# Optimization experiments

Hardware: AMD Instinct MI355X
Metric: run time of the kernel (lower is better)

Reference implementation:

```python
import jax, jax.numpy as jnp
import numpy as np

HEADS = 4
KD = 32          # key_dim per head
LEVELS = 2
G = 3            # 2**dims - 1 HP orientation groups
STRENGTH = 0.25
DECAY = 0.6
LN_EPS = 1e-5
MIX_EPS = 1e-3


def _layernorm(x, g, b):
    m = jnp.mean(x, axis=-1, keepdims=True)
    v = jnp.var(x, axis=-1, keepdims=True)
    return (x - m) * jax.lax.rsqrt(v + LN_EPS) * g + b


def _dwt2(x):
    # Haar analysis, periodic/even sizes. [B,H,W,C] -> [B,H/2,W/2,4C] (LL,LH,HL,HH)
    x00 = x[:, 0::2, 0::2]; x01 = x[:, 0::2, 1::2]
    x10 = x[:, 1::2, 0::2]; x11 = x[:, 1::2, 1::2]
    ll = (x00 + x01 + x10 + x11) * 0.5
    lh = (x00 - x01 + x10 - x11) * 0.5
    hl = (x00 + x01 - x10 - x11) * 0.5
    hh = (x00 - x01 - x10 + x11) * 0.5
    return jnp.concatenate([ll, lh, hl, hh], axis=-1)


def _idwt2(w):
    # exact Haar synthesis: [B,H/2,W/2,4C] -> [B,H,W,C]
    ll, lh, hl, hh = jnp.split(w, 4, axis=-1)
    x00 = (ll + lh + hl + hh) * 0.5
    x01 = (ll - lh + hl - hh) * 0.5
    x10 = (ll + lh - hl - hh) * 0.5
    x11 = (ll - lh - hl + hh) * 0.5
    B, H2, W2, C = ll.shape
    r0 = jnp.stack([x00, x01], axis=3).reshape(B, H2, 2 * W2, C)  # interleave W
    r1 = jnp.stack([x10, x11], axis=3).reshape(B, H2, 2 * W2, C)
    return jnp.stack([r0, r1], axis=2).reshape(B, 2 * H2, 2 * W2, C)  # interleave H


def _axial_mhsa(x, p):
    # AxialMHSAND: sequential sweep over spatial axes; each pass is
    # proj(attn(softmax(QK^T/sqrt(d)) V)) on norm(x), qkv via 1x1 conv (=matmul).
    g, b, wq, bq, wk, bk, wv, bv, wp, bp = p
    scale = KD ** -0.5
    for axis in (1, 2):
        X = _layernorm(x, g, b)
        B, H, W, _ = X.shape
        Q = (X @ wq + bq).reshape(B, H, W, HEADS, KD)
        K = (X @ wk + bk).reshape(B, H, W, HEADS, KD)
        V = (X @ wv + bv).reshape(B, H, W, HEADS, KD)
        if axis == 1:  # attend along H, batch over (B, W, heads)
            A = jax.nn.softmax(jnp.einsum('bqwnd,bkwnd->bwnqk', Q, K) * scale, axis=-1)
            Y = jnp.einsum('bwnqk,bkwnd->bqwnd', A, V)
        else:          # attend along W, batch over (B, H, heads)
            A = jax.nn.softmax(jnp.einsum('bhqnd,bhknd->bhnqk', Q, K) * scale, axis=-1)
            Y = jnp.einsum('bhnqk,bhknd->bhqnd', A, V)
        x = Y.reshape(B, H, W, HEADS * KD) @ wp + bp
    return x


def setup_inputs() -> dict:
    key = jax.random.key(0)
    ks = jax.random.split(key, 24)
    C = 64
    HD = HEADS * KD
    s = 0.02
    inp = {'x': jax.random.normal(ks[0], (4, 256, 256, C), jnp.float32)}
    i = 1
    for pre in ('lp', 'hp'):
        inp[pre + '_ln_g'] = jnp.ones((C,), jnp.float32)
        inp[pre + '_ln_b'] = jnp.zeros((C,), jnp.float32)
        inp[pre + '_wq'] = jax.random.normal(ks[i], (C, HD), jnp.float32) * s
        inp[pre + '_bq'] = jax.random.normal(ks[i + 1], (HD,), jnp.float32) * s
        inp[pre + '_wk'] = jax.random.normal(ks[i + 2], (C, HD), jnp.float32) * s
        inp[pre + '_bk'] = jax.random.normal(ks[i + 3], (HD,), jnp.float32) * s
        inp[pre + '_wv'] = jax.random.normal(ks[i + 4], (C, HD), jnp.float32) * s
        inp[pre + '_bv'] = jax.random.normal(ks[i + 5], (HD,), jnp.float32) * s
        inp[pre + '_wp'] = jax.random.normal(ks[i + 6], (HD, C), jnp.float32) * s
        inp[pre + '_bp'] = jax.random.normal(ks[i + 7], (C,), jnp.float32) * s
        i += 8
    mix = jnp.eye(G, dtype=jnp.float32) + MIX_EPS * (jnp.ones((G, G), jnp.float32) - jnp.eye(G, dtype=jnp.float32))
    inp['mix_w0'] = mix
    inp['mix_w1'] = mix
    return inp


def reference(x, lp_ln_g, lp_ln_b, lp_wq, lp_bq, lp_wk, lp_bk, lp_wv, lp_bv, lp_wp, lp_bp,
              hp_ln_g, hp_ln_b, hp_wq, hp_bq, hp_wk, hp_bk, hp_wv, hp_bv, hp_wp, hp_bp,
              mix_w0, mix_w1):
    lp_p = (lp_ln_g, lp_ln_b, lp_wq, lp_bq, lp_wk, lp_bk, lp_wv, lp_bv, lp_wp, lp_bp)
    hp_p = (hp_ln_g, hp_ln_b, hp_wq, hp_bq, hp_wk, hp_bk, hp_wv, hp_bv, hp_wp, hp_bp)
    mix_ws = [mix_w0, mix_w1]
    C = x.shape[-1]
    cur = x
    hps = []
    for _ in range(LEVELS):  # analysis pyramid
        w = _dwt2(cur)
        hps.append(w[..., C:])
        cur = w[..., :C]
    # deepest LP: axial attention, residual with full strength
    cur = cur + STRENGTH * _axial_mhsa(cur, lp_p)
    for l in reversed(range(LEVELS)):  # synthesis with per-level HP processing
        hp = hps[l]
        B, H2, W2, _ = hp.shape
        gain = STRENGTH * (DECAY ** (LEVELS - 1 - l))  # coarser levels stronger
        hp_g = hp.reshape(B, H2, W2, G, C)
        mixed = jnp.einsum('gd,bhwdc->bhwgc', mix_ws[l], hp_g)  # OrientationMix
        batched = mixed.transpose(3, 0, 1, 2, 4).reshape(G * B, H2, W2, C)
        att = _axial_mhsa(batched, hp_p)  # shared hp_attn across groups/levels
        att = att.reshape(G, B, H2, W2, C).transpose(1, 2, 3, 0, 4).reshape(B, H2, W2, G * C)
        hp_out = hp + gain * att
        cur = _idwt2(jnp.concatenate([cur, hp_out], axis=-1))
    return cur
```

## Files before the change

kernel.cpp:

```cpp
#include <hip/hip_runtime.h>

#define LN_EPS 1e-5f
#define QSCALE 0.25500526578425445f

typedef __attribute__((ext_vector_type(8))) short bf16x8;
typedef __attribute__((ext_vector_type(4))) float f32x4;

#define MFMA16(A, B, C) __builtin_amdgcn_mfma_f32_16x16x32_bf16(A, B, C, 0, 0, 0)

static __device__ __forceinline__ unsigned short f2bf_rne(float f) {
    union { unsigned int i; float f; } c; c.f = f;
    unsigned int i = c.i;
    return (unsigned short)((i + 0x7fffu + ((i >> 16) & 1u)) >> 16);
}
static __device__ __forceinline__ void bfstore2(unsigned short* p, float x, float y) {
    *(unsigned int*)p = (unsigned int)f2bf_rne(x) | ((unsigned int)f2bf_rne(y) << 16);
}
static __device__ __forceinline__ unsigned pk2(float a, float b) {
    return __builtin_amdgcn_perm(__builtin_bit_cast(unsigned, b),
                                 __builtin_bit_cast(unsigned, a), 0x07060302u);
}
static __device__ __forceinline__ unsigned short tb16(float f) {
    return (unsigned short)(__builtin_bit_cast(unsigned, f) >> 16);
}
static __device__ __forceinline__ float bftrunc(float f) {
    return __builtin_bit_cast(float, __builtin_bit_cast(unsigned, f) & 0xFFFF0000u);
}

__global__ void dwt_kernel(const float4* __restrict__ in, float4* __restrict__ ll,
                           float4* __restrict__ hp, int B, int H2, int W2) {
    const int i = blockIdx.x * blockDim.x + threadIdx.x;
    const int total = B * H2 * W2 * 16;
    if (i >= total) return;
    const int c4 = i & 15;
    int t = i >> 4;
    const int w2 = t % W2; t /= W2;
    const int h2 = t % H2;
    const int b = t / H2;
    const int W = W2 * 2;
    const size_t base = (((size_t)b * (H2 * 2) + 2 * h2) * W + 2 * w2) * 16 + c4;
    const float4 x00 = in[base];
    const float4 x01 = in[base + 16];
    const float4 x10 = in[base + (size_t)W * 16];
    const float4 x11 = in[base + (size_t)W * 16 + 16];
    float4 vll, vlh, vhl, vhh;
#define DWTC(a) \
    vll.a = (x00.a + x01.a + x10.a + x11.a) * 0.5f; \
    vlh.a = (x00.a - x01.a + x10.a - x11.a) * 0.5f; \
    vhl.a = (x00.a + x01.a - x10.a - x11.a) * 0.5f; \
    vhh.a = (x00.a - x01.a - x10.a + x11.a) * 0.5f;
    DWTC(x) DWTC(y) DWTC(z) DWTC(w)
#undef DWTC
    const size_t oi = ((size_t)b * H2 + h2) * W2 + w2;
    ll[oi * 16 + c4] = vll;
    hp[oi * 48 + c4] = vlh;
    hp[oi * 48 + 16 + c4] = vhl;
    hp[oi * 48 + 32 + c4] = vhh;
}

__global__ void idwt_kernel(const float4* __restrict__ cur, const float4* __restrict__ hp,
                            const float4* __restrict__ att, float gain,
                            float4* __restrict__ out, int B, int H2, int W2) {
    const int i = blockIdx.x * blockDim.x + threadIdx.x;
    const int total = B * H2 * W2 * 16;
    if (i >= total) return;
    const int c4 = i & 15;
    int t = i >> 4;
    const int w2 = t % W2; t /= W2;
    const int h2 = t % H2;
    const int b = t / H2;
    const size_t oi = ((size_t)b * H2 + h2) * W2 + w2;
    const size_t sp = (size_t)h2 * W2 + w2;
    const size_t gstr = (size_t)B * H2 * W2;
    const float4 vll = cur[oi * 16 + c4];
    float4 vlh = hp[oi * 48 + c4];
    float4 vhl = hp[oi * 48 + 16 + c4];
    float4 vhh = hp[oi * 48 + 32 + c4];
    const float4 a0 = att[((size_t)b * H2 * W2 + sp) * 16 + c4];
    const float4 a1 = att[((size_t)b * H2 * W2 + gstr + sp) * 16 + c4];
    const float4 a2 = att[((size_t)b * H2 * W2 + 2 * gstr + sp) * 16 + c4];
#define ADDG(a) \
    vlh.a = fmaf(gain, a0.a, vlh.a); \
    vhl.a = fmaf(gain, a1.a, vhl.a); \
    vhh.a = fmaf(gain, a2.a, vhh.a);
    ADDG(x) ADDG(y) ADDG(z) ADDG(w)
#undef ADDG
    float4 x00, x01, x10, x11;
#define IDWTC(a) \
    x00.a = (vll.a + vlh.a + vhl.a + vhh.a) * 0.5f; \
    x01.a = (vll.a - vlh.a + vhl.a - vhh.a) * 0.5f; \
    x10.a = (vll.a + vlh.a - vhl.a - vhh.a) * 0.5f; \
    x11.a = (vll.a - vlh.a - vhl.a + vhh.a) * 0.5f;
    IDWTC(x) IDWTC(y) IDWTC(z) IDWTC(w)
#undef IDWTC
    const int W = W2 * 2;
    const size_t r0 = (((size_t)b * (H2 * 2) + 2 * h2) * W + 2 * w2) * 16 + c4;
    out[r0] = x00;
    out[r0 + 16] = x01;
    out[r0 + (size_t)W * 16] = x10;
    out[r0 + (size_t)W * 16 + 16] = x11;
}

__global__ void prep_weights(const float* __restrict__ lwq, const float* __restrict__ lwk,
                             const float* __restrict__ lwv, const float* __restrict__ lwp,
                             const float* __restrict__ hwq, const float* __restrict__ hwk,
                             const float* __restrict__ hwv, const float* __restrict__ hwp,
                             unsigned short* __restrict__ wbuf) {
    const int i = blockIdx.x * blockDim.x + threadIdx.x;
    if (i >= 65536) return;
    const int set = i >> 15;
    const int r = i & 32767;
    const float* wq = set ? hwq : lwq;
    const float* wk = set ? hwk : lwk;
    const float* wv = set ? hwv : lwv;
    const float* wp = set ? hwp : lwp;
    float v;
    if (r < 24576) {
        const int nn = r >> 6, c = r & 63;
        const float* w = (nn < 128) ? wq : (nn < 256) ? wk : wv;
        v = w[c * 128 + (nn & 127)];
        if (nn < 128) v *= QSCALE;
    } else {
        const int r2 = r - 24576;
        const int nn = r2 >> 7, d = r2 & 127;
        v = wp[d * 64 + nn];
    }
    wbuf[i] = f2bf_rne(v);
}

struct Job {
    const float* xin;
    const float* mixsrc;
    const float* mixw;
    float* xout;
    const float* basep;
    float res_scale;
    const float* ln_g; const float* ln_b;
    const float* bq; const float* bk; const float* bv; const float* bp;
    const unsigned short* wqkvT;
    const unsigned short* wpT;
};

template<int S>
__global__ __launch_bounds__(512, 4)
void axial_attn(Job jA, Job jB, int nA, int axis)
{
    constexpr int BS = 512;
    constexpr int CK = 32;
    constexpr int NCH = S / CK;
    constexpr int NSI = S / 32;
    constexpr int CSTR = 40;

    __shared__ __align__(16) unsigned short Xs[S * 64];
    __shared__ __align__(16) unsigned short Arena[18432];

    const int tid = threadIdx.x;
    const int lane = tid & 63;
    const int w = tid >> 6;
    const int n16 = lane & 15;
    const int quad = lane >> 4;

    const bool isB = (int)blockIdx.x >= nA;
    const Job j = isB ? jB : jA;
    const int line = isB ? (int)blockIdx.x - nA : (int)blockIdx.x;
    const int lb = line / S;
    const int lr = line - lb * S;
    size_t lbase, tstr;
    if (axis == 1) { lbase = ((size_t)lb * S * S + lr) * 64; tstr = (size_t)S * 64; }
    else           { lbase = ((size_t)lb * S + lr) * (size_t)S * 64; tstr = 64; }

    const bf16x8 Wk0 = *(const bf16x8*)&j.wqkvT[((8 + w) * 16 + n16) * 64 + quad * 8];
    const bf16x8 Wk1 = *(const bf16x8*)&j.wqkvT[((8 + w) * 16 + n16) * 64 + 32 + quad * 8];
    const bf16x8 Wv0 = *(const bf16x8*)&j.wqkvT[((16 + w) * 16 + n16) * 64 + quad * 8];
    const bf16x8 Wv1 = *(const bf16x8*)&j.wqkvT[((16 + w) * 16 + n16) * 64 + 32 + quad * 8];
    const float bk = j.bk[w * 16 + n16];
    const float bv = j.bv[w * 16 + n16];

    {
        const int sub = tid & 15;
        const float4 g4 = ((const float4*)j.ln_g)[sub];
        const float4 be4 = ((const float4*)j.ln_b)[sub];
        const float4* x4 = (const float4*)j.xin;
        const float4* hp4 = (const float4*)j.mixsrc;
        const size_t lbase4 = lbase >> 2, tstr4 = tstr >> 2;
        float m0, m1, m2; int bimg;
        if (hp4) {
            const int g = lb >> 2;
            bimg = lb & 3;
            m0 = j.mixw[g * 3 + 0]; m1 = j.mixw[g * 3 + 1]; m2 = j.mixw[g * 3 + 2];
        }
        for (int t = (tid >> 4); t < S; t += BS / 16) {
            float4 v;
            if (hp4) {
                const int pos = (axis == 1) ? (t * S + lr) : (lr * S + t);
                const size_t hb = ((size_t)bimg * S * S + pos) * 48 + sub;
                const float4 h0 = hp4[hb];
                const float4 h1 = hp4[hb + 16];
                const float4 h2 = hp4[hb + 32];
                v.x = m0 * h0.x + m1 * h1.x + m2 * h2.x;
                v.y = m0 * h0.y + m1 * h1.y + m2 * h2.y;
                v.z = m0 * h0.z + m1 * h1.z + m2 * h2.z;
                v.w = m0 * h0.w + m1 * h1.w + m2 * h2.w;
            } else {
                v = x4[lbase4 + (size_t)t * tstr4 + sub];
            }
            float s = v.x + v.y + v.z + v.w;
            float ss = v.x * v.x + v.y * v.y + v.z * v.z + v.w * v.w;
            #pragma unroll
            for (int m = 1; m < 16; m <<= 1) {
                s += __shfl_xor(s, m);
                ss += __shfl_xor(ss, m);
            }
            const float mean = s * 0.015625f;
            const float rstd = rsqrtf(ss * 0.015625f - mean * mean + LN_EPS);
            unsigned short* xr = &Xs[(t << 6) + ((sub * 4) ^ ((t & 7) << 3))];
            bfstore2(xr,     (v.x - mean) * rstd * g4.x + be4.x,
                             (v.y - mean) * rstd * g4.y + be4.y);
            bfstore2(xr + 2, (v.z - mean) * rstd * g4.z + be4.z,
                             (v.w - mean) * rstd * g4.w + be4.w);
        }
    }
    __syncthreads();

    {
        const float bias = j.bq[w * 16 + n16] * QSCALE;
        const bf16x8 Bq0 = *(const bf16x8*)&j.wqkvT[(w * 16 + n16) * 64 + quad * 8];
        const bf16x8 Bq1 = *(const bf16x8*)&j.wqkvT[(w * 16 + n16) * 64 + 32 + quad * 8];
        #pragma unroll
        for (int mt = 0; mt < S / 16; ++mt) {
            const int xr = mt * 16 + n16;
            const int xm = (xr & 7) << 3;
            const bf16x8 A0 = *(const bf16x8*)&Xs[(xr << 6) + ((quad * 8) ^ xm)];
            const bf16x8 A1 = *(const bf16x8*)&Xs[(xr << 6) + ((32 + quad * 8) ^ xm)];
            f32x4 acc = {bias, bias, bias, bias};
            acc = MFMA16(A0, Bq0, acc);
            acc = MFMA16(A1, Bq1, acc);
            const int row0 = mt * 16 + quad * 4;
            #pragma unroll
            for (int r = 0; r < 4; ++r) {
                const int rr = row0 + r;
                Arena[(rr << 7) + ((w * 16 + n16) ^ ((rr & 7) << 3))] = tb16(acc[r]);
            }
        }
    }
    __syncthreads();

    const int h = w >> 1;
    const int sub = w & 1;
    const int hoff = h * 32;

    bf16x8 qb[NSI];
    #pragma unroll
    for (int si = 0; si < NSI; ++si) {
        const int qr = (sub * NSI + si) * 16 + n16;
        qb[si] = *(const bf16x8*)&Arena[(qr << 7) + ((hoff + quad * 8) ^ ((qr & 7) << 3))];
    }
    f32x4 y0[NSI], y1[NSI];
    float rsum[NSI];
    #pragma unroll
    for (int si = 0; si < NSI; ++si) {
        y0[si] = (f32x4){0.f, 0.f, 0.f, 0.f};
        y1[si] = (f32x4){0.f, 0.f, 0.f, 0.f};
        rsum[si] = 0.f;
    }
    __syncthreads();

    auto produce = [&](int kc, int buf) {
        const int k0 = kc * CK;
        unsigned short* Kc = &Arena[buf * 4096];
        unsigned short* Vc = &Arena[8192 + buf * 5120];
        #pragma unroll
        for (int mtl = 0; mtl < 2; ++mtl) {
            const int xr = k0 + mtl * 16 + n16;
            const int xm = (xr & 7) << 3;
            const bf16x8 A0 = *(const bf16x8*)&Xs[(xr << 6) + ((quad * 8) ^ xm)];
            const bf16x8 A1 = *(const bf16x8*)&Xs[(xr << 6) + ((32 + quad * 8) ^ xm)];
            f32x4 ak = {bk, bk, bk, bk};
            ak = MFMA16(A0, Wk0, ak);
            ak = MFMA16(A1, Wk1, ak);
            const int row0 = mtl * 16 + quad * 4;
            #pragma unroll
            for (int r = 0; r < 4; ++r) {
                const int rr = row0 + r;
                Kc[(rr << 7) + ((w * 16 + n16) ^ ((rr & 7) << 3))] = tb16(ak[r]);
            }
            f32x4 av = {bv, bv, bv, bv};
            av = MFMA16(A0, Wv0, av);
            av = MFMA16(A1, Wv1, av);
            *(uint2*)&Vc[(w * 16 + n16) * CSTR + mtl * 16 + quad * 4] =
                make_uint2(pk2(av[0], av[1]), pk2(av[2], av[3]));
        }
    };

    const int sr0 = ((n16 >> 2) << 3) + (n16 & 3);
    const int sr1 = sr0 + 4;

    produce(0, 0);
    __syncthreads();
    for (int kc = 0; kc < NCH; ++kc) {
        const int buf = kc & 1;
        const unsigned short* Kc = &Arena[buf * 4096];
        const unsigned short* Vc = &Arena[8192 + buf * 5120];
        const bf16x8 ka0 = *(const bf16x8*)&Kc[(sr0 << 7) + ((hoff + quad * 8) ^ ((sr0 & 7) << 3))];
        const bf16x8 ka1 = *(const bf16x8*)&Kc[(sr1 << 7) + ((hoff + quad * 8) ^ ((sr1 & 7) << 3))];
        const bf16x8 vb0 = *(const bf16x8*)&Vc[(hoff + n16) * CSTR + quad * 8];
        const bf16x8 vb1 = *(const bf16x8*)&Vc[(hoff + 16 + n16) * CSTR + quad * 8];
        if (kc + 1 < NCH) produce(kc + 1, buf ^ 1);
        #pragma unroll
        for (int si = 0; si < NSI; ++si) {
            f32x4 sc0 = {0.f, 0.f, 0.f, 0.f};
            f32x4 sc1 = {0.f, 0.f, 0.f, 0.f};
            sc0 = MFMA16(ka0, qb[si], sc0);
            sc1 = MFMA16(ka1, qb[si], sc1);
            const float e0 = __builtin_amdgcn_exp2f(sc0[0]);
            const float e1 = __builtin_amdgcn_exp2f(sc0[1]);
            const float e2 = __builtin_amdgcn_exp2f(sc0[2]);
            const float e3 = __builtin_amdgcn_exp2f(sc0[3]);
            const float e4 = __builtin_amdgcn_exp2f(sc1[0]);
            const float e5 = __builtin_amdgcn_exp2f(sc1[1]);
            const float e6 = __builtin_amdgcn_exp2f(sc1[2]);
            const float e7 = __builtin_amdgcn_exp2f(sc1[3]);
            rsum[si] += ((bftrunc(e0) + bftrunc(e1)) + (bftrunc(e2) + bftrunc(e3)))
                      + ((bftrunc(e4) + bftrunc(e5)) + (bftrunc(e6) + bftrunc(e7)));
            union { unsigned u[4]; bf16x8 v; } pau;
            pau.u[0] = pk2(e0, e1);
            pau.u[1] = pk2(e2, e3);
            pau.u[2] = pk2(e4, e5);
            pau.u[3] = pk2(e6, e7);
            y0[si] = MFMA16(pau.v, vb0, y0[si]);
            y1[si] = MFMA16(pau.v, vb1, y1[si]);
        }
        __syncthreads();
    }

    #pragma unroll
    for (int si = 0; si < NSI; ++si) {
        float red = rsum[si];
        red += __shfl_xor(red, 16);
        red += __shfl_xor(red, 32);
        const int q0 = (sub * NSI + si) * 16;
        #pragma unroll
        for (int r = 0; r < 4; ++r) {
            const float inv = __builtin_amdgcn_rcpf(__shfl(red, quad * 4 + r));
            const int row = q0 + quad * 4 + r;
            const int m = (row & 7) << 3;
            Arena[(row << 7) + ((hoff + n16) ^ m)]      = tb16(y0[si][r] * inv);
            Arena[(row << 7) + ((hoff + 16 + n16) ^ m)] = tb16(y1[si][r] * inv);
        }
    }
    __syncthreads();

    {
        constexpr int TD = (S / 16) * 4 / 8;
        const int mt = (w * TD) >> 2;
        const int nt0 = (w * TD) & 3;
        const int m0 = mt * 16;
        const int ym = (n16 & 7) << 3;
        bf16x8 pa[4];
        #pragma unroll
        for (int kt = 0; kt < 4; ++kt)
            pa[kt] = *(const bf16x8*)&Arena[((m0 + n16) << 7) + ((kt * 32 + quad * 8) ^ ym)];
        #pragma unroll
        for (int i = 0; i < TD; ++i) {
            const int nt = nt0 + i;
            const float bias = j.bp[nt * 16 + n16];
            f32x4 acc = {bias, bias, bias, bias};
            #pragma unroll
            for (int kt = 0; kt < 4; ++kt) {
                const bf16x8 wb = *(const bf16x8*)&j.wpT[(nt * 16 + n16) * 128 + kt * 32 + quad * 8];
                acc = MFMA16(pa[kt], wb, acc);
            }
            #pragma unroll
            for (int r = 0; r < 4; ++r) {
                const size_t gi = lbase + (size_t)(m0 + quad * 4 + r) * tstr + nt * 16 + n16;
                float v = acc[r];
                if (j.basep) v = fmaf(j.res_scale, v, j.basep[gi]);
                j.xout[gi] = v;
            }
        }
    }
}

extern "C" void kernel_launch(void* const* d_in, const int* in_sizes, int n_in,
                              void* d_out, int out_size, void* d_ws, size_t ws_size,
                              hipStream_t stream) {
    (void)in_sizes; (void)n_in; (void)out_size; (void)ws_size;
    const float* x = (const float*)d_in[0];
    const float* P_lp[10];
    const float* P_hp[10];
    for (int i = 0; i < 10; ++i) P_lp[i] = (const float*)d_in[1 + i];
    for (int i = 0; i < 10; ++i) P_hp[i] = (const float*)d_in[11 + i];
    const float* mw0 = (const float*)d_in[21];
    const float* mw1 = (const float*)d_in[22];
    float* out = (float*)d_out;
    float* ws = (float*)d_ws;

    float* ll0 = ws;
    float* hp0 = ll0 + (size_t)4194304;
    float* t0  = hp0 + (size_t)12582912;
    float* ll1  = t0;
    float* hp1  = t0 + (size_t)1048576;
    float* ta2  = t0 + (size_t)4194304;
    float* lpta = t0 + (size_t)7340032;
    float* tb  = out;
    float* t1b = out;
    unsigned short* wbuf = (unsigned short*)(out + (size_t)13631488);

    prep_weights<<<256, 256, 0, stream>>>(
        P_lp[2], P_lp[4], P_lp[6], P_lp[8],
        P_hp[2], P_hp[4], P_hp[6], P_hp[8], wbuf);

    dwt_kernel<<<4 * 128 * 128 * 16 / 256, 256, 0, stream>>>(
        (const float4*)x, (float4*)ll0, (float4*)hp0, 4, 128, 128);
    dwt_kernel<<<4 * 64 * 64 * 16 / 256, 256, 0, stream>>>(
        (const float4*)ll0, (float4*)ll1, (float4*)hp1, 4, 64, 64);

    const unsigned short* lp_qkvT = wbuf;
    const unsigned short* lp_wpT  = wbuf + 24576;
    const unsigned short* hp_qkvT = wbuf + 32768;
    const unsigned short* hp_wpT  = wbuf + 32768 + 24576;

    auto mkjob = [](const float* xin, const float* mixsrc, const float* mixw,
                    float* xout, const float* basep, float rs,
                    const float* const* P, const unsigned short* qkvT,
                    const unsigned short* wpT) {
        Job jj;
        jj.xin = xin; jj.mixsrc = mixsrc; jj.mixw = mixw;
        jj.xout = xout; jj.basep = basep; jj.res_scale = rs;
        jj.ln_g = P[0]; jj.ln_b = P[1];
        jj.bq = P[3]; jj.bk = P[5]; jj.bv = P[7]; jj.bp = P[9];
        jj.wqkvT = qkvT; jj.wpT = wpT;
        return jj;
    };

    {
        Job a1 = mkjob(ll1, nullptr, nullptr, lpta, nullptr, 1.f, P_lp, lp_qkvT, lp_wpT);
        Job b1 = mkjob(nullptr, hp1, mw1, tb, nullptr, 1.f, P_hp, hp_qkvT, hp_wpT);
        axial_attn<64><<<1024, 512, 0, stream>>>(a1, b1, 256, 1);
        Job a2 = mkjob(lpta, nullptr, nullptr, ll1, ll1, 0.25f, P_lp, lp_qkvT, lp_wpT);
        Job b2 = mkjob(tb, nullptr, nullptr, ta2, nullptr, 1.f, P_hp, hp_qkvT, hp_wpT);
        axial_attn<64><<<1024, 512, 0, stream>>>(a2, b2, 256, 2);
    }
    idwt_kernel<<<4 * 64 * 64 * 16 / 256, 256, 0, stream>>>(
        (const float4*)ll1, (const float4*)hp1, (const float4*)ta2, 0.25f,
        (float4*)ll0, 4, 64, 64);

    {
        Job c1 = mkjob(nullptr, hp0, mw0, t1b, nullptr, 1.f, P_hp, hp_qkvT, hp_wpT);
        axial_attn<128><<<1536, 512, 0, stream>>>(c1, c1, 1536, 1);
        Job c2 = mkjob(t1b, nullptr, nullptr, t0, nullptr, 1.f, P_hp, hp_qkvT, hp_wpT);
        axial_attn<128><<<1536, 512, 0, stream>>>(c2, c2, 1536, 2);
    }
    idwt_kernel<<<4 * 128 * 128 * 16 / 256, 256, 0, stream>>>(
        (const float4*)ll0, (const float4*)hp0, (const float4*)t0, 0.15f,
        (float4*)out, 4, 128, 128);
}
```

Measured before the change: 398.6 us.

## Make each wave compute its own head's Q/K/V to drop block barriers

Each wave now projects Q, K and V only for its own head's 32 columns into a private shared-memory slice. This replaces the shared, double-buffered K/V production that needed a block-wide __syncthreads per chunk. The waves sharing a head now compute the same K/V redundantly, which doubles K/V MFMA work, and the produce step no longer overlaps with attention. The Y staging buffer moves to a padded row layout in place of the XOR swizzle.

After: 467.8 us. +17.4%, slower.

```diff
diff --git a/kernel.cpp b/kernel.cpp
--- a/kernel.cpp
+++ b/kernel.cpp
@@ -146,13 +146,12 @@
 void axial_attn(Job jA, Job jB, int nA, int axis)
 {
     constexpr int BS = 512;
-    constexpr int CK = 32;
-    constexpr int NCH = S / CK;
     constexpr int NSI = S / 32;
-    constexpr int CSTR = 40;
+    constexpr int NCH = S / 32;
+    constexpr int SLICE = 2304;
 
     __shared__ __align__(16) unsigned short Xs[S * 64];
-    __shared__ __align__(16) unsigned short Arena[18432];
+    __shared__ __align__(16) unsigned short Arena[8 * SLICE];
 
     const int tid = threadIdx.x;
     const int lane = tid & 63;
@@ -169,12 +168,12 @@
     if (axis == 1) { lbase = ((size_t)lb * S * S + lr) * 64; tstr = (size_t)S * 64; }
     else           { lbase = ((size_t)lb * S + lr) * (size_t)S * 64; tstr = 64; }
 
-    const bf16x8 Wk0 = *(const bf16x8*)&j.wqkvT[((8 + w) * 16 + n16) * 64 + quad * 8];
-    const bf16x8 Wk1 = *(const bf16x8*)&j.wqkvT[((8 + w) * 16 + n16) * 64 + 32 + quad * 8];
-    const bf16x8 Wv0 = *(const bf16x8*)&j.wqkvT[((16 + w) * 16 + n16) * 64 + quad * 8];
-    const bf16x8 Wv1 = *(const bf16x8*)&j.wqkvT[((16 + w) * 16 + n16) * 64 + 32 + quad * 8];
-    const float bk = j.bk[w * 16 + n16];
-    const float bv = j.bv[w * 16 + n16];
+    const int hh = w >> 1;
+    const int qhalf = w & 1;
+    const int qbase = qhalf * (S / 2);
+    unsigned short* Qw = &Arena[w * SLICE];
+    unsigned short* Kw = &Arena[w * SLICE];
+    unsigned short* Vw = &Arena[w * SLICE + 1024];
 
     {
         const int sub = tid & 15;
@@ -222,39 +221,40 @@
     }
     __syncthreads();
 
-    {
-        const float bias = j.bq[w * 16 + n16] * QSCALE;
-        const bf16x8 Bq0 = *(const bf16x8*)&j.wqkvT[(w * 16 + n16) * 64 + quad * 8];
-        const bf16x8 Bq1 = *(const bf16x8*)&j.wqkvT[(w * 16 + n16) * 64 + 32 + quad * 8];
-        #pragma unroll
-        for (int mt = 0; mt < S / 16; ++mt) {
-            const int xr = mt * 16 + n16;
-            const int xm = (xr & 7) << 3;
-            const bf16x8 A0 = *(const bf16x8*)&Xs[(xr << 6) + ((quad * 8) ^ xm)];
-            const bf16x8 A1 = *(const bf16x8*)&Xs[(xr << 6) + ((32 + quad * 8) ^ xm)];
+    #pragma unroll
+    for (int si = 0; si < NSI; ++si) {
+        const int xr = qbase + si * 16 + n16;
+        const int xm = (xr & 7) << 3;
+        const bf16x8 A0 = *(const bf16x8*)&Xs[(xr << 6) + ((quad * 8) ^ xm)];
+        const bf16x8 A1 = *(const bf16x8*)&Xs[(xr << 6) + ((32 + quad * 8) ^ xm)];
+        #pragma unroll
+        for (int c = 0; c < 2; ++c) {
+            const int nt = 2 * hh + c;
+            const float bias = j.bq[nt * 16 + n16] * QSCALE;
+            const bf16x8 B0 = *(const bf16x8*)&j.wqkvT[(nt * 16 + n16) * 64 + quad * 8];
+            const bf16x8 B1 = *(const bf16x8*)&j.wqkvT[(nt * 16 + n16) * 64 + 32 + quad * 8];
             f32x4 acc = {bias, bias, bias, bias};
-            acc = MFMA16(A0, Bq0, acc);
-            acc = MFMA16(A1, Bq1, acc);
-            const int row0 = mt * 16 + quad * 4;
+            acc = MFMA16(A0, B0, acc);
+            acc = MFMA16(A1, B1, acc);
             #pragma unroll
             for (int r = 0; r < 4; ++r) {
-                const int rr = row0 + r;
-                Arena[(rr << 7) + ((w * 16 + n16) ^ ((rr & 7) << 3))] = tb16(acc[r]);
-            }
-        }
-    }
-    __syncthreads();
-
-    const int h = w >> 1;
-    const int sub = w & 1;
-    const int hoff = h * 32;
+                const int lrow = si * 16 + quad * 4 + r;
+                const int col = c * 16 + n16;
+                Qw[lrow * 32 + ((((col >> 3) ^ (lrow & 3)) << 3) | (col & 7))] = tb16(acc[r]);
+            }
+        }
+    }
+    asm volatile("s_waitcnt lgkmcnt(0)" ::: "memory");
 
     bf16x8 qb[NSI];
     #pragma unroll
     for (int si = 0; si < NSI; ++si) {
-        const int qr = (sub * NSI + si) * 16 + n16;
-        qb[si] = *(const bf16x8*)&Arena[(qr << 7) + ((hoff + quad * 8) ^ ((qr & 7) << 3))];
-    }
+        const int lrow = si * 16 + n16;
+        qb[si] = *(const bf16x8*)&Qw[lrow * 32 + ((quad ^ (lrow & 3)) << 3)];
+    }
+    asm volatile("s_waitcnt lgkmcnt(0)" ::: "memory");
+    __builtin_amdgcn_sched_barrier(0);
+
     f32x4 y0[NSI], y1[NSI];
     float rsum[NSI];
     #pragma unroll
@@ -263,49 +263,59 @@
         y1[si] = (f32x4){0.f, 0.f, 0.f, 0.f};
         rsum[si] = 0.f;
     }
-    __syncthreads();
-
-    auto produce = [&](int kc, int buf) {
-        const int k0 = kc * CK;
-        unsigned short* Kc = &Arena[buf * 4096];
-        unsigned short* Vc = &Arena[8192 + buf * 5120];
+    const int sr0 = ((n16 >> 2) << 3) + (n16 & 3);
+    const int sr1 = sr0 + 4;
+
+    for (int kc = 0; kc < NCH; ++kc) {
+        const int k0 = kc * 32;
+        bf16x8 A[2][2];
         #pragma unroll
         for (int mtl = 0; mtl < 2; ++mtl) {
             const int xr = k0 + mtl * 16 + n16;
             const int xm = (xr & 7) << 3;
-            const bf16x8 A0 = *(const bf16x8*)&Xs[(xr << 6) + ((quad * 8) ^ xm)];
-            const bf16x8 A1 = *(const bf16x8*)&Xs[(xr << 6) + ((32 + quad * 8) ^ xm)];
-            f32x4 ak = {bk, bk, bk, bk};
-            ak = MFMA16(A0, Wk0, ak);
-            ak = MFMA16(A1, Wk1, ak);
-            const int row0 = mtl * 16 + quad * 4;
-            #pragma unroll
-            for (int r = 0; r < 4; ++r) {
-                const int rr = row0 + r;
-                Kc[(rr << 7) + ((w * 16 + n16) ^ ((rr & 7) << 3))] = tb16(ak[r]);
-            }
-            f32x4 av = {bv, bv, bv, bv};
-            av = MFMA16(A0, Wv0, av);
-            av = MFMA16(A1, Wv1, av);
-            *(uint2*)&Vc[(w * 16 + n16) * CSTR + mtl * 16 + quad * 4] =
-                make_uint2(pk2(av[0], av[1]), pk2(av[2], av[3]));
-        }
-    };
-
-    const int sr0 = ((n16 >> 2) << 3) + (n16 & 3);
-    const int sr1 = sr0 + 4;
-
-    produce(0, 0);
-    __syncthreads();
-    for (int kc = 0; kc < NCH; ++kc) {
-        const int buf = kc & 1;
-        const unsigned short* Kc = &Arena[buf * 4096];
-        const unsigned short* Vc = &Arena[8192 + buf * 5120];
-        const bf16x8 ka0 = *(const bf16x8*)&Kc[(sr0 << 7) + ((hoff + quad * 8) ^ ((sr0 & 7) << 3))];
-        const bf16x8 ka1 = *(const bf16x8*)&Kc[(sr1 << 7) + ((hoff + quad * 8) ^ ((sr1 & 7) << 3))];
-        const bf16x8 vb0 = *(const bf16x8*)&Vc[(hoff + n16) * CSTR + quad * 8];
-        const bf16x8 vb1 = *(const bf16x8*)&Vc[(hoff + 16 + n16) * CSTR + quad * 8];
-        if (kc + 1 < NCH) produce(kc + 1, buf ^ 1);
+            A[mtl][0] = *(const bf16x8*)&Xs[(xr << 6) + ((quad * 8) ^ xm)];
+            A[mtl][1] = *(const bf16x8*)&Xs[(xr << 6) + ((32 + quad * 8) ^ xm)];
+        }
+        #pragma unroll
+        for (int c = 0; c < 2; ++c) {
+            const int nt = 8 + 2 * hh + c;
+            const float bias = j.bk[(2 * hh + c) * 16 + n16];
+            const bf16x8 W0 = *(const bf16x8*)&j.wqkvT[(nt * 16 + n16) * 64 + quad * 8];
+            const bf16x8 W1 = *(const bf16x8*)&j.wqkvT[(nt * 16 + n16) * 64 + 32 + quad * 8];
+            #pragma unroll
+            for (int mtl = 0; mtl < 2; ++mtl) {
+                f32x4 ak = {bias, bias, bias, bias};
+                ak = MFMA16(A[mtl][0], W0, ak);
+                ak = MFMA16(A[mtl][1], W1, ak);
+                #pragma unroll
+                for (int r = 0; r < 4; ++r) {
+                    const int key = mtl * 16 + quad * 4 + r;
+                    const int col = c * 16 + n16;
+                    Kw[key * 32 + ((((col >> 3) ^ (key & 3)) << 3) | (col & 7))] = tb16(ak[r]);
+                }
+            }
+        }
+        #pragma unroll
+        for (int c = 0; c < 2; ++c) {
+            const int nt = 16 + 2 * hh + c;
+            const float bias = j.bv[(2 * hh + c) * 16 + n16];
+            const bf16x8 W0 = *(const bf16x8*)&j.wqkvT[(nt * 16 + n16) * 64 + quad * 8];
+            const bf16x8 W1 = *(const bf16x8*)&j.wqkvT[(nt * 16 + n16) * 64 + 32 + quad * 8];
+            #pragma unroll
+            for (int mtl = 0; mtl < 2; ++mtl) {
+                f32x4 av = {bias, bias, bias, bias};
+                av = MFMA16(A[mtl][0], W0, av);
+                av = MFMA16(A[mtl][1], W1, av);
+                *(uint2*)&Vw[(c * 16 + n16) * 40 + mtl * 16 + quad * 4] =
+                    make_uint2(pk2(av[0], av[1]), pk2(av[2], av[3]));
+            }
+        }
+        asm volatile("s_waitcnt lgkmcnt(0)" ::: "memory");
+        __builtin_amdgcn_sched_barrier(0);
+        const bf16x8 ka0 = *(const bf16x8*)&Kw[sr0 * 32 + ((quad ^ (sr0 & 3)) << 3)];
+        const bf16x8 ka1 = *(const bf16x8*)&Kw[sr1 * 32 + ((quad ^ (sr1 & 3)) << 3)];
+        const bf16x8 vb0 = *(const bf16x8*)&Vw[n16 * 40 + quad * 8];
+        const bf16x8 vb1 = *(const bf16x8*)&Vw[(16 + n16) * 40 + quad * 8];
         #pragma unroll
         for (int si = 0; si < NSI; ++si) {
             f32x4 sc0 = {0.f, 0.f, 0.f, 0.f};
@@ -330,22 +340,22 @@
             y0[si] = MFMA16(pau.v, vb0, y0[si]);
             y1[si] = MFMA16(pau.v, vb1, y1[si]);
         }
-        __syncthreads();
-    }
-
+    }
+
+    __syncthreads();
+
+    unsigned short* Yst = Arena;
     #pragma unroll
     for (int si = 0; si < NSI; ++si) {
         float red = rsum[si];
         red += __shfl_xor(red, 16);
         red += __shfl_xor(red, 32);
-        const int q0 = (sub * NSI + si) * 16;
         #pragma unroll
         for (int r = 0; r < 4; ++r) {
             const float inv = __builtin_amdgcn_rcpf(__shfl(red, quad * 4 + r));
-            const int row = q0 + quad * 4 + r;
-            const int m = (row & 7) << 3;
-            Arena[(row << 7) + ((hoff + n16) ^ m)]      = tb16(y0[si][r] * inv);
-            Arena[(row << 7) + ((hoff + 16 + n16) ^ m)] = tb16(y1[si][r] * inv);
+            const int grow = qbase + si * 16 + quad * 4 + r;
+            Yst[grow * 136 + 32 * hh + n16]      = tb16(y0[si][r] * inv);
+            Yst[grow * 136 + 32 * hh + 16 + n16] = tb16(y1[si][r] * inv);
         }
     }
     __syncthreads();
@@ -355,11 +365,10 @@
         const int mt = (w * TD) >> 2;
         const int nt0 = (w * TD) & 3;
         const int m0 = mt * 16;
-        const int ym = (n16 & 7) << 3;
         bf16x8 pa[4];
         #pragma unroll
         for (int kt = 0; kt < 4; ++kt)
-            pa[kt] = *(const bf16x8*)&Arena[((m0 + n16) << 7) + ((kt * 32 + quad * 8) ^ ym)];
+            pa[kt] = *(const bf16x8*)&Yst[(m0 + n16) * 136 + kt * 32 + quad * 8];
         #pragma unroll
         for (int i = 0; i < TD; ++i) {
             const int nt = nt0 + i;
```
